# Optimization experiments

Measured on AMD Instinct MI355X. Metric: run time of the kernel, lower is better.

The kernel has to match this reference:

```python
import jax, jax.numpy as jnp
import numpy as np

BN_EPS = 1e-5


def setup_inputs() -> dict:
    key = jax.random.key(0)
    ks = jax.random.split(key, 8)
    N, H, OUT = 32 * 1024, 512, 32
    return {
        "x": jax.random.normal(ks[0], (N, 2), dtype=jnp.float32),
        "batch_size": 32,
        "Wq": jax.random.normal(ks[1], (2, H), dtype=jnp.float32) / np.sqrt(2.0),
        "Wk": jax.random.normal(ks[2], (2, H), dtype=jnp.float32) / np.sqrt(2.0),
        "Wv": jax.random.normal(ks[3], (2, H), dtype=jnp.float32) / np.sqrt(2.0),
        "bn_gamma": jnp.ones((H,), jnp.float32),
        "bn_beta": jnp.zeros((H,), jnp.float32),
        "bn_mean": jnp.zeros((H,), jnp.float32),
        "bn_var": jnp.ones((H,), jnp.float32),
        "prelu_a": jnp.full((1,), 0.25, jnp.float32),
        "W_out": jax.random.normal(ks[4], (H, OUT), dtype=jnp.float32) / np.sqrt(H),
        "b_out": jnp.zeros((OUT,), jnp.float32),
    }


def reference(x, batch_size, Wq, Wk, Wv, bn_gamma, bn_beta, bn_mean, bn_var,
              prelu_a, W_out, b_out):
    H = Wq.shape[1]
    # project tokens [N,2] -> [B,S,H]
    q = (x @ Wq).reshape(batch_size, -1, H)
    k = (x @ Wk).reshape(batch_size, -1, H)
    v = (x @ Wv).reshape(batch_size, -1, H)
    scale = 1.0 / jnp.sqrt(jnp.asarray(H, x.dtype))
    attn = jax.nn.softmax(jnp.einsum("bqh,bkh->bqk", q, k) * scale, axis=-1)
    out = jnp.einsum("bqk,bkh->bqh", attn, v).reshape(-1, H)  # [N,H]
    # BatchNorm1d (eval mode) + PReLU + Linear (dropout = identity in eval)
    out = (out - bn_mean) * (bn_gamma / jnp.sqrt(bn_var + BN_EPS)) + bn_beta
    out = jnp.where(out >= 0, out, prelu_a[0] * out)
    return out @ W_out + b_out
```

## Files before the change

kernel.cpp:

```cpp
#include <hip/hip_runtime.h>
#include <math.h>


#define H_DIM   512
#define OUT_DIM 32
#define S_LEN   1024
#define THREADS 256
#define NW 4

#if __has_builtin(__builtin_amdgcn_exp2f)
#define EXP2(x) __builtin_amdgcn_exp2f(x)
#else
#define EXP2(x) exp2f(x)
#endif

typedef __attribute__((ext_vector_type(8))) short bf16x8;
typedef __attribute__((ext_vector_type(4))) float f32x4;

__device__ __forceinline__ unsigned int rne_bf16(float f) {
    unsigned int u = __float_as_uint(f);
    return (u + 0x7fffu + ((u >> 16) & 1u)) >> 16;
}
__device__ __forceinline__ unsigned int pack2bf16(float lo, float hi) {
    return rne_bf16(lo) | (rne_bf16(hi) << 16);
}

union frag_cast { unsigned int u[4]; int4 i4; bf16x8 v; };

__global__ __launch_bounds__(THREADS)
void fused_attn_kernel(const float* __restrict__ x,
                       const float* __restrict__ Wq,
                       const float* __restrict__ Wk,
                       const float* __restrict__ Wv,
                       const float* __restrict__ bn_gamma,
                       const float* __restrict__ bn_beta,
                       const float* __restrict__ bn_mean,
                       const float* __restrict__ bn_var,
                       const float* __restrict__ prelu_a,
                       const float* __restrict__ Wout,
                       const float* __restrict__ bout,
                       float* __restrict__ out)
{
    __shared__ float2 xs[S_LEN];
    __shared__ float4 abcs[H_DIM];
    __shared__ unsigned int bfr[32 * 64 * 4];
    __shared__ float redl[NW][64], redw0[NW][64], redw1[NW][64];
    __shared__ float mred[NW][4];

    const int t    = threadIdx.x;
    const int lane = t & 63;
    const int q    = __builtin_amdgcn_readfirstlane(t >> 6);
    const int b    = blockIdx.x >> 4;
    const int tile = blockIdx.x & 15;
    const float scale = 0.044194173824159216f;
    const float L2E   = 1.4426950408889634f;

    const float4* xg = (const float4*)(x + (size_t)b * (S_LEN * 2));
    float4* xs4 = (float4*)xs;
    xs4[t]       = xg[t];
    xs4[t + 256] = xg[t + 256];

    #pragma unroll
    for (int k = 0; k < 2; ++k) {
        int h = t + k * 256;
        float g = bn_gamma[h] * rsqrtf(bn_var[h] + 1e-5f);
        abcs[h] = make_float4(Wv[h] * g, Wv[H_DIM + h] * g,
                              bn_beta[h] - bn_mean[h] * g, 0.f);
    }

    {
        float m00 = 0.f, m01 = 0.f, m10 = 0.f, m11 = 0.f;
        #pragma unroll
        for (int k = 0; k < 2; ++k) {
            int h = t + k * 256;
            float a0 = Wq[h], a1 = Wq[H_DIM + h];
            float b0 = Wk[h], b1 = Wk[H_DIM + h];
            m00 = fmaf(a0, b0, m00); m01 = fmaf(a0, b1, m01);
            m10 = fmaf(a1, b0, m10); m11 = fmaf(a1, b1, m11);
        }
        #pragma unroll
        for (int off = 32; off >= 1; off >>= 1) {
            m00 += __shfl_xor(m00, off); m01 += __shfl_xor(m01, off);
            m10 += __shfl_xor(m10, off); m11 += __shfl_xor(m11, off);
        }
        if (lane == 0) {
            mred[q][0] = m00; mred[q][1] = m01;
            mred[q][2] = m10; mred[q][3] = m11;
        }
    }

    #pragma unroll
    for (int k = 0; k < 32; ++k) {
        int i    = k * 256 + t;
        int c    = i & 15;
        int jj   = (i >> 4) & 3;
        int quad = (i >> 6) & 3;
        int s    = (i >> 8) & 15;
        int nt   = (i >> 12) & 1;
        int h    = s * 32 + quad * 8 + 2 * jj;
        int o    = nt * 16 + c;
        float f0 = Wout[h * 32 + o];
        float f1 = Wout[(h + 1) * 32 + o];
        int F = (nt * 16 + s) * 256 + (quad * 16 + c) * 4 + jj;
        bfr[F] = pack2bf16(f0, f1);
    }
    __syncthreads();

    float m00 = (mred[0][0] + mred[1][0] + mred[2][0] + mred[3][0]) * scale;
    float m01 = (mred[0][1] + mred[1][1] + mred[2][1] + mred[3][1]) * scale;
    float m10 = (mred[0][2] + mred[1][2] + mred[2][2] + mred[3][2]) * scale;
    float m11 = (mred[0][3] + mred[1][3] + mred[2][3] + mred[3][3]) * scale;

    const float2 xt = xs[tile * 64 + lane];
    const float u0L = fmaf(xt.x, m00, xt.y * m10) * L2E;
    const float u1L = fmaf(xt.x, m01, xt.y * m11) * L2E;

    float l = 0.f, w0 = 0.f, w1 = 0.f;
    const float4* kv = ((const float4*)xs) + q * 128;
    #pragma unroll 4
    for (int i = 0; i < 128; ++i) {
        float4 k2 = kv[i];
        float e0 = EXP2(fmaf(u0L, k2.x, u1L * k2.y));
        float e1 = EXP2(fmaf(u0L, k2.z, u1L * k2.w));
        l += e0 + e1;
        w0 = fmaf(e0, k2.x, fmaf(e1, k2.z, w0));
        w1 = fmaf(e0, k2.y, fmaf(e1, k2.w, w1));
    }
    redl[q][lane] = l; redw0[q][lane] = w0; redw1[q][lane] = w1;
    __syncthreads();
    l  = redl[0][lane]  + redl[1][lane]  + redl[2][lane]  + redl[3][lane];
    w0 = redw0[0][lane] + redw0[1][lane] + redw0[2][lane] + redw0[3][lane];
    w1 = redw1[0][lane] + redw1[1][lane] + redw1[2][lane] + redw1[3][lane];
    const float inv = 1.0f / l;
    w0 *= inv; w1 *= inv;

    const int src = q * 16 + (lane & 15);
    const float w0t = __shfl(w0, src);
    const float w1t = __shfl(w1, src);

    const float ap = prelu_a[0];
    const int quad = lane >> 4;
    f32x4 acc0 = {0.f, 0.f, 0.f, 0.f};
    f32x4 acc1 = {0.f, 0.f, 0.f, 0.f};
    const int4* bsrc = (const int4*)bfr;

    for (int s = 0; s < 16; ++s) {
        frag_cast bf0, bf1;
        bf0.i4 = bsrc[s * 64 + lane];
        bf1.i4 = bsrc[(16 + s) * 64 + lane];
        const int hbase = s * 32 + quad * 8;
        frag_cast af;
        #pragma unroll
        for (int jj = 0; jj < 4; ++jj) {
            float4 c0 = abcs[hbase + jj * 2];
            float4 c1 = abcs[hbase + jj * 2 + 1];
            float z0 = fmaf(w0t, c0.x, fmaf(w1t, c0.y, c0.z));
            float z1 = fmaf(w0t, c1.x, fmaf(w1t, c1.y, c1.z));
            float p0 = fmaxf(z0, 0.f) + ap * fminf(z0, 0.f);
            float p1 = fmaxf(z1, 0.f) + ap * fminf(z1, 0.f);
            af.u[jj] = pack2bf16(p0, p1);
        }
        acc0 = __builtin_amdgcn_mfma_f32_16x16x32_bf16(af.v, bf0.v, acc0, 0, 0, 0);
        acc1 = __builtin_amdgcn_mfma_f32_16x16x32_bf16(af.v, bf1.v, acc1, 0, 0, 0);
    }

    const size_t base = (size_t)(b * S_LEN + tile * 64) * OUT_DIM;
    const int o0 = lane & 15;
    const float bo0 = bout[o0], bo1 = bout[16 + o0];
    #pragma unroll
    for (int r = 0; r < 4; ++r) {
        const int tt = q * 16 + quad * 4 + r;
        out[base + tt * 32 + o0]      = acc0[r] + bo0;
        out[base + tt * 32 + 16 + o0] = acc1[r] + bo1;
    }
}

extern "C" void kernel_launch(void* const* d_in, const int* in_sizes, int n_in,
                              void* d_out, int out_size, void* d_ws, size_t ws_size,
                              hipStream_t stream) {
    const float* x    = (const float*)d_in[0];
    const float* Wq   = (const float*)d_in[2];
    const float* Wk   = (const float*)d_in[3];
    const float* Wv   = (const float*)d_in[4];
    const float* gam  = (const float*)d_in[5];
    const float* bet  = (const float*)d_in[6];
    const float* mean = (const float*)d_in[7];
    const float* var  = (const float*)d_in[8];
    const float* pa   = (const float*)d_in[9];
    const float* Wout = (const float*)d_in[10];
    const float* bo   = (const float*)d_in[11];
    float* out = (float*)d_out;

    const int N = in_sizes[0] / 2;
    const int blocks = N / 64;
    hipLaunchKernelGGL(fused_attn_kernel, dim3(blocks), dim3(THREADS), 0, stream,
                       x, Wq, Wk, Wv, gam, bet, mean, var, pa, Wout, bo, out);
}
```

Baseline: 93.38 us.

## Use packed FP32 math, hardware bf16 convert, and SoA shared layouts

Splits the shared x tile into separate x and y arrays and repacks the BN/Wv constants so the inner loops can use two-wide packed FMAs. The softmax accumulation loop and the BN+PReLU epilogue now run on float2 vectors. PReLU is rewritten as a blend of z and |z|, and the manual round-to-nearest bf16 packing is replaced by the v_cvt_pk_bf16_f32 instruction. The aim is to cut VALU instruction count in the exp loop and the epilogue. In exchange it relies on inline asm for this target and may round slightly differently.

```diff
diff --git a/kernel.cpp b/kernel.cpp
--- a/kernel.cpp
+++ b/kernel.cpp
@@ -16,13 +16,15 @@
 
 typedef __attribute__((ext_vector_type(8))) short bf16x8;
 typedef __attribute__((ext_vector_type(4))) float f32x4;
-
-__device__ __forceinline__ unsigned int rne_bf16(float f) {
-    unsigned int u = __float_as_uint(f);
-    return (u + 0x7fffu + ((u >> 16) & 1u)) >> 16;
-}
-__device__ __forceinline__ unsigned int pack2bf16(float lo, float hi) {
-    return rne_bf16(lo) | (rne_bf16(hi) << 16);
+typedef __attribute__((ext_vector_type(2))) float f32x2;
+
+__device__ __forceinline__ f32x2 pkfma(f32x2 a, f32x2 b, f32x2 c) {
+    return __builtin_elementwise_fma(a, b, c);
+}
+__device__ __forceinline__ unsigned int cvt_pk_bf16(float lo, float hi) {
+    unsigned int r;
+    asm("v_cvt_pk_bf16_f32 %0, %1, %2" : "=v"(r) : "v"(lo), "v"(hi));
+    return r;
 }
 
 union frag_cast { unsigned int u[4]; int4 i4; bf16x8 v; };
@@ -41,8 +43,10 @@
                        const float* __restrict__ bout,
                        float* __restrict__ out)
 {
-    __shared__ float2 xs[S_LEN];
-    __shared__ float4 abcs[H_DIM];
+    __shared__ __align__(16) float xsx[S_LEN];
+    __shared__ __align__(16) float xsy[S_LEN];
+    __shared__ float4 a01s[H_DIM / 2];
+    __shared__ float2 cps[H_DIM / 2];
     __shared__ unsigned int bfr[32 * 64 * 4];
     __shared__ float redl[NW][64], redw0[NW][64], redw1[NW][64];
     __shared__ float mred[NW][4];
@@ -56,16 +60,28 @@
     const float L2E   = 1.4426950408889634f;
 
     const float4* xg = (const float4*)(x + (size_t)b * (S_LEN * 2));
-    float4* xs4 = (float4*)xs;
-    xs4[t]       = xg[t];
-    xs4[t + 256] = xg[t + 256];
-
-    #pragma unroll
-    for (int k = 0; k < 2; ++k) {
-        int h = t + k * 256;
-        float g = bn_gamma[h] * rsqrtf(bn_var[h] + 1e-5f);
-        abcs[h] = make_float4(Wv[h] * g, Wv[H_DIM + h] * g,
-                              bn_beta[h] - bn_mean[h] * g, 0.f);
+    f32x2* xsx2 = (f32x2*)xsx;
+    f32x2* xsy2 = (f32x2*)xsy;
+    {
+        float4 v0 = xg[t];
+        float4 v1 = xg[t + 256];
+        f32x2 a = {v0.x, v0.z}; xsx2[t] = a;
+        f32x2 c = {v0.y, v0.w}; xsy2[t] = c;
+        f32x2 d = {v1.x, v1.z}; xsx2[t + 256] = d;
+        f32x2 e = {v1.y, v1.w}; xsy2[t + 256] = e;
+    }
+
+    {
+        const float2 gm = ((const float2*)bn_gamma)[t];
+        const float2 vr = ((const float2*)bn_var)[t];
+        const float2 bt = ((const float2*)bn_beta)[t];
+        const float2 mn = ((const float2*)bn_mean)[t];
+        const float2 wv0 = ((const float2*)Wv)[t];
+        const float2 wv1 = ((const float2*)(Wv + H_DIM))[t];
+        float g0 = gm.x * rsqrtf(vr.x + 1e-5f);
+        float g1 = gm.y * rsqrtf(vr.y + 1e-5f);
+        a01s[t] = make_float4(wv0.x * g0, wv0.y * g1, wv1.x * g0, wv1.y * g1);
+        cps[t]  = make_float2(bt.x - mn.x * g0, bt.y - mn.y * g1);
     }
 
     {
@@ -102,7 +118,7 @@
         float f0 = Wout[h * 32 + o];
         float f1 = Wout[(h + 1) * 32 + o];
         int F = (nt * 16 + s) * 256 + (quad * 16 + c) * 4 + jj;
-        bfr[F] = pack2bf16(f0, f1);
+        bfr[F] = cvt_pk_bf16(f0, f1);
     }
     __syncthreads();
 
@@ -111,21 +127,39 @@
     float m10 = (mred[0][2] + mred[1][2] + mred[2][2] + mred[3][2]) * scale;
     float m11 = (mred[0][3] + mred[1][3] + mred[2][3] + mred[3][3]) * scale;
 
-    const float2 xt = xs[tile * 64 + lane];
-    const float u0L = fmaf(xt.x, m00, xt.y * m10) * L2E;
-    const float u1L = fmaf(xt.x, m01, xt.y * m11) * L2E;
-
-    float l = 0.f, w0 = 0.f, w1 = 0.f;
-    const float4* kv = ((const float4*)xs) + q * 128;
+    const float xtx = xsx[tile * 64 + lane];
+    const float xty = xsy[tile * 64 + lane];
+    const float u0L = fmaf(xtx, m00, xty * m10) * L2E;
+    const float u1L = fmaf(xtx, m01, xty * m11) * L2E;
+    const f32x2 u0L2 = {u0L, u0L};
+    const f32x2 u1L2 = {u1L, u1L};
+
+    f32x2 l2  = {0.f, 0.f};
+    f32x2 w02 = {0.f, 0.f};
+    f32x2 w12 = {0.f, 0.f};
+    const float4* kx4 = (const float4*)(xsx + q * 256);
+    const float4* ky4 = (const float4*)(xsy + q * 256);
     #pragma unroll 4
-    for (int i = 0; i < 128; ++i) {
-        float4 k2 = kv[i];
-        float e0 = EXP2(fmaf(u0L, k2.x, u1L * k2.y));
-        float e1 = EXP2(fmaf(u0L, k2.z, u1L * k2.w));
-        l += e0 + e1;
-        w0 = fmaf(e0, k2.x, fmaf(e1, k2.z, w0));
-        w1 = fmaf(e0, k2.y, fmaf(e1, k2.w, w1));
-    }
+    for (int i = 0; i < 64; ++i) {
+        float4 kx = kx4[i];
+        float4 ky = ky4[i];
+        f32x2 kxa = {kx.x, kx.y};
+        f32x2 kxb = {kx.z, kx.w};
+        f32x2 kya = {ky.x, ky.y};
+        f32x2 kyb = {ky.z, ky.w};
+        f32x2 arga = pkfma(u0L2, kxa, u1L2 * kya);
+        f32x2 argb = pkfma(u0L2, kxb, u1L2 * kyb);
+        f32x2 ea = {EXP2(arga.x), EXP2(arga.y)};
+        f32x2 eb = {EXP2(argb.x), EXP2(argb.y)};
+        l2  = l2 + ea + eb;
+        w02 = pkfma(ea, kxa, w02);
+        w02 = pkfma(eb, kxb, w02);
+        w12 = pkfma(ea, kya, w12);
+        w12 = pkfma(eb, kyb, w12);
+    }
+    float l  = l2.x + l2.y;
+    float w0 = w02.x + w02.y;
+    float w1 = w12.x + w12.y;
     redl[q][lane] = l; redw0[q][lane] = w0; redw1[q][lane] = w1;
     __syncthreads();
     l  = redl[0][lane]  + redl[1][lane]  + redl[2][lane]  + redl[3][lane];
@@ -137,8 +171,12 @@
     const int src = q * 16 + (lane & 15);
     const float w0t = __shfl(w0, src);
     const float w1t = __shfl(w1, src);
+    const f32x2 w0t2 = {w0t, w0t};
+    const f32x2 w1t2 = {w1t, w1t};
 
     const float ap = prelu_a[0];
+    const f32x2 ca2 = {0.5f * (1.f + ap), 0.5f * (1.f + ap)};
+    const f32x2 cb2 = {0.5f * (1.f - ap), 0.5f * (1.f - ap)};
     const int quad = lane >> 4;
     f32x4 acc0 = {0.f, 0.f, 0.f, 0.f};
     f32x4 acc1 = {0.f, 0.f, 0.f, 0.f};
@@ -148,17 +186,19 @@
         frag_cast bf0, bf1;
         bf0.i4 = bsrc[s * 64 + lane];
         bf1.i4 = bsrc[(16 + s) * 64 + lane];
-        const int hbase = s * 32 + quad * 8;
+        const int hb2 = s * 16 + quad * 4;
         frag_cast af;
         #pragma unroll
         for (int jj = 0; jj < 4; ++jj) {
-            float4 c0 = abcs[hbase + jj * 2];
-            float4 c1 = abcs[hbase + jj * 2 + 1];
-            float z0 = fmaf(w0t, c0.x, fmaf(w1t, c0.y, c0.z));
-            float z1 = fmaf(w0t, c1.x, fmaf(w1t, c1.y, c1.z));
-            float p0 = fmaxf(z0, 0.f) + ap * fminf(z0, 0.f);
-            float p1 = fmaxf(z1, 0.f) + ap * fminf(z1, 0.f);
-            af.u[jj] = pack2bf16(p0, p1);
+            float4 a = a01s[hb2 + jj];
+            float2 c = cps[hb2 + jj];
+            f32x2 a0 = {a.x, a.y};
+            f32x2 a1 = {a.z, a.w};
+            f32x2 cc = {c.x, c.y};
+            f32x2 z  = pkfma(w0t2, a0, pkfma(w1t2, a1, cc));
+            f32x2 az = __builtin_elementwise_abs(z);
+            f32x2 p  = pkfma(ca2, z, cb2 * az);
+            af.u[jj] = cvt_pk_bf16(p.x, p.y);
         }
         acc0 = __builtin_amdgcn_mfma_f32_16x16x32_bf16(af.v, bf0.v, acc0, 0, 0, 0);
         acc1 = __builtin_amdgcn_mfma_f32_16x16x32_bf16(af.v, bf1.v, acc1, 0, 0, 0);
```

Measured after the change: 87.93 us. 5.8% less time.
